# Kernel tuning notes

Measured on AMD Instinct MI355X. Metric: run time of the kernel, lower is better.

The kernel has to match this reference:

```python
import jax, jax.numpy as jnp
import numpy as np

D_MODEL = 1024
N_HEADS = 16
D_K = D_MODEL // N_HEADS
NEG = -1e9


def setup_inputs() -> dict:
    key = jax.random.key(0)
    ks = jax.random.split(key, 10)
    B, S = 4, 2048
    x = jax.random.normal(ks[0], (B, S, D_MODEL), dtype=jnp.float32)
    mask = jax.random.randint(ks[1], (B, S, S), 0, 2).astype(jnp.bool_)
    sc = 1.0 / np.sqrt(D_MODEL)
    Wq = jax.random.normal(ks[2], (D_MODEL, D_MODEL), dtype=jnp.float32) * sc
    bq = jnp.zeros((D_MODEL,), dtype=jnp.float32)
    Wk = jax.random.normal(ks[3], (D_MODEL, D_MODEL), dtype=jnp.float32) * sc
    bk = jnp.zeros((D_MODEL,), dtype=jnp.float32)
    Wv = jax.random.normal(ks[4], (D_MODEL, D_MODEL), dtype=jnp.float32) * sc
    bv = jnp.zeros((D_MODEL,), dtype=jnp.float32)
    Wo = jax.random.normal(ks[5], (D_MODEL, D_MODEL), dtype=jnp.float32) * sc
    bo = jnp.zeros((D_MODEL,), dtype=jnp.float32)
    return {"x": x, "mask": mask, "Wq": Wq, "bq": bq, "Wk": Wk, "bk": bk,
            "Wv": Wv, "bv": bv, "Wo": Wo, "bo": bo}


def _split_heads(t, B, S):
    # [B,S,d_model] -> [B,H,S,d_k]
    return t.reshape(B, S, N_HEADS, D_K).transpose(0, 2, 1, 3)


def reference(x, mask, Wq, bq, Wk, bk, Wv, bv, Wo, bo):
    B, S, _ = x.shape
    Q = _split_heads(x @ Wq + bq, B, S)
    K = _split_heads(x @ Wk + bk, B, S)
    V = _split_heads(x @ Wv + bv, B, S)
    scale = jnp.sqrt(jnp.float32(D_K))
    scores = jnp.einsum('bhqd,bhkd->bhqk', Q, K) / scale
    scores = jnp.where(mask[:, None, :, :], jnp.float32(NEG), scores)
    attn = jax.nn.softmax(scores, axis=-1)
    ctx = jnp.einsum('bhqk,bhkd->bhqd', attn, V)
    ctx = ctx.transpose(0, 2, 1, 3).reshape(B, S, D_MODEL)
    return ctx @ Wo + bo
```

## Files before the change

kernel.cpp:

```cpp
#include <hip/hip_runtime.h>

#define D_MODEL 1024
#define N_HEADS 16
#define D_K     64
#define BATCH   4
#define SEQ     2048
#define MROWS   (BATCH * SEQ)

typedef __bf16 bf16x8 __attribute__((ext_vector_type(8)));
typedef float  f32x4  __attribute__((ext_vector_type(4)));
typedef unsigned short ushort8 __attribute__((ext_vector_type(8)));
typedef unsigned short ushort4v __attribute__((ext_vector_type(4)));

__device__ inline unsigned short f2bf(float f) {
    union { float f; unsigned int u; } v; v.f = f;
    unsigned int u = v.u;
    unsigned int r = (u + 0x7fffu + ((u >> 16) & 1u)) >> 16;
    return (unsigned short)r;
}

__device__ inline void load_lds16(const void* g, void* l) {
    __builtin_amdgcn_global_load_lds(
        (const __attribute__((address_space(1))) unsigned int*)g,
        (__attribute__((address_space(3))) unsigned int*)l, 16, 0, 0);
}

__global__ __launch_bounds__(256) void wprep(const float* __restrict__ Wq,
                                             const float* __restrict__ Wk,
                                             const float* __restrict__ Wv,
                                             const float* __restrict__ Wo,
                                             unsigned short* __restrict__ wt) {
    __shared__ __align__(16) unsigned short t[64][65];
    int w  = blockIdx.z;
    const float* W = (w == 0) ? Wq : (w == 1) ? Wk : (w == 2) ? Wv : Wo;
    int k0 = blockIdx.x * 64, n0 = blockIdx.y * 64;
    int tid = threadIdx.x;
    int nl = tid & 63, kq = tid >> 6;
#pragma unroll
    for (int i = 0; i < 16; i++) {
        int kl = kq * 16 + i;
        t[kl][nl] = f2bf(W[(size_t)(k0 + kl) * D_MODEL + n0 + nl]);
    }
    __syncthreads();
    unsigned short* out = wt + (size_t)w * D_MODEL * D_MODEL;
#pragma unroll
    for (int p = 0; p < 2; p++) {
        int nrow = p * 32 + (tid >> 3);
        int c8   = (tid & 7) * 8;
        ushort8 o;
#pragma unroll
        for (int j = 0; j < 8; j++) o[j] = t[c8 + j][nrow];
        *reinterpret_cast<ushort8*>(out + (size_t)(n0 + nrow) * D_MODEL + k0 + c8) = o;
    }
}

__global__ __launch_bounds__(256) void xprep(const float4* __restrict__ x,
                                             unsigned short* __restrict__ xb) {
    int i = blockIdx.x * 256 + threadIdx.x;
    float4 v = x[i];
    ushort4v o;
    o[0] = f2bf(v.x); o[1] = f2bf(v.y); o[2] = f2bf(v.z); o[3] = f2bf(v.w);
    *reinterpret_cast<ushort4v*>(xb + (size_t)i * 4) = o;
}

__global__ __launch_bounds__(256) void mprep(const int* __restrict__ mask,
                                             unsigned long long* __restrict__ mb) {
    int row = blockIdx.x;
    int tid = threadIdx.x;
    int wv  = tid >> 6;
#pragma unroll
    for (int w = 0; w < 8; w++) {
        int col = w * 256 + tid;
        int mval = mask[(size_t)row * SEQ + col];
        unsigned long long bits = __ballot(mval != 0);
        if ((tid & 63) == 0) mb[(size_t)row * 32 + w * 4 + wv] = bits;
    }
}

__global__ __launch_bounds__(256) void qkv_gemm(const unsigned short* __restrict__ xb,
                                                const unsigned short* __restrict__ wt,
                                                const float* __restrict__ bq,
                                                const float* __restrict__ bk,
                                                const float* __restrict__ bvv,
                                                unsigned short* __restrict__ qb,
                                                unsigned short* __restrict__ kb,
                                                unsigned short* __restrict__ vt) {
    __shared__ __align__(16) unsigned short lds_a[128 * 32];
    __shared__ __align__(16) unsigned short lds_b[128 * 32];
    int tid = threadIdx.x;
    int wave = tid >> 6, lane = tid & 63;
    int c = lane & 15, g = lane >> 4;
    int wave_m = (wave & 1) * 64, wave_n = (wave >> 1) * 64;
    int nblk = blockIdx.x * 128, mblk = blockIdx.y * 128;

    int oct0 = wave * 128 + lane, oct1 = oct0 + 64;
    int ra0 = oct0 >> 2, ga0 = ((oct0 & 3) ^ (ra0 & 3)) * 8;
    int ra1 = oct1 >> 2, ga1 = ((oct1 & 3) ^ (ra1 & 3)) * 8;
    const unsigned short* pa0 = xb + (size_t)(mblk + ra0) * D_MODEL + ga0;
    const unsigned short* pa1 = xb + (size_t)(mblk + ra1) * D_MODEL + ga1;
    const unsigned short* pb0 = wt + (size_t)(nblk + ra0) * D_MODEL + ga0;
    const unsigned short* pb1 = wt + (size_t)(nblk + ra1) * D_MODEL + ga1;
    unsigned short* la0 = lds_a + wave * 1024;
    unsigned short* la1 = la0 + 512;
    unsigned short* lb0 = lds_b + wave * 1024;
    unsigned short* lb1 = lb0 + 512;

    int aoff[4], boff[4];
#pragma unroll
    for (int mi = 0; mi < 4; mi++) {
        int row = wave_m + mi * 16 + c;
        aoff[mi] = (row * 4 + (g ^ (row & 3))) * 16;
    }
#pragma unroll
    for (int ni = 0; ni < 4; ni++) {
        int row = wave_n + ni * 16 + c;
        boff[ni] = (row * 4 + (g ^ (row & 3))) * 16;
    }

    f32x4 acc[4][4];
#pragma unroll
    for (int mi = 0; mi < 4; mi++)
#pragma unroll
        for (int ni = 0; ni < 4; ni++) acc[mi][ni] = f32x4{0.f, 0.f, 0.f, 0.f};

    for (int k0 = 0; k0 < D_MODEL; k0 += 32) {
        load_lds16(pa0 + k0, la0);
        load_lds16(pa1 + k0, la1);
        load_lds16(pb0 + k0, lb0);
        load_lds16(pb1 + k0, lb1);
        __syncthreads();
        bf16x8 af[4], bfr[4];
#pragma unroll
        for (int mi = 0; mi < 4; mi++)
            af[mi] = *reinterpret_cast<const bf16x8*>(reinterpret_cast<const char*>(lds_a) + aoff[mi]);
#pragma unroll
        for (int ni = 0; ni < 4; ni++)
            bfr[ni] = *reinterpret_cast<const bf16x8*>(reinterpret_cast<const char*>(lds_b) + boff[ni]);
#pragma unroll
        for (int mi = 0; mi < 4; mi++)
#pragma unroll
            for (int ni = 0; ni < 4; ni++)
                acc[mi][ni] = __builtin_amdgcn_mfma_f32_16x16x32_bf16(af[mi], bfr[ni], acc[mi][ni], 0, 0, 0);
        __syncthreads();
    }

    int nb = nblk + wave_n;
    int wsel = nb >> 10;
    int h = (nb >> 6) & 15;
    int dk0 = nb & 63;
    int mglob = mblk + wave_m;
    int b = mglob >> 11;
    int s0 = mglob & (SEQ - 1);
    size_t bh = (size_t)(b * N_HEADS + h);
    const float* bias = (wsel == 0) ? bq : (wsel == 1) ? bk : bvv;
    int nn = nb & (D_MODEL - 1);
    float bval[4];
#pragma unroll
    for (int ni = 0; ni < 4; ni++) bval[ni] = bias[nn + ni * 16 + c];

    if (wsel < 2) {
        unsigned short* outp = wsel ? kb : qb;
#pragma unroll
        for (int mi = 0; mi < 4; mi++)
#pragma unroll
            for (int ni = 0; ni < 4; ni++) {
                int dk = dk0 + ni * 16 + c;
#pragma unroll
                for (int r = 0; r < 4; r++) {
                    int s = s0 + mi * 16 + g * 4 + r;
                    outp[(bh * SEQ + s) * 64 + dk] = f2bf(acc[mi][ni][r] + bval[ni]);
                }
            }
    } else {
#pragma unroll
        for (int mi = 0; mi < 4; mi++)
#pragma unroll
            for (int ni = 0; ni < 4; ni++) {
                int dk = dk0 + ni * 16 + c;
                int s = s0 + mi * 16 + g * 4;
                ushort4v o;
#pragma unroll
                for (int r = 0; r < 4; r++) o[r] = f2bf(acc[mi][ni][r] + bval[ni]);
                *reinterpret_cast<ushort4v*>(vt + (bh * 64 + dk) * SEQ + s) = o;
            }
    }
}

__global__ __launch_bounds__(256) void attn(const unsigned short* __restrict__ qb,
                                            const unsigned short* __restrict__ kb,
                                            const unsigned short* __restrict__ vt,
                                            const unsigned long long* __restrict__ mb,
                                            unsigned short* __restrict__ ctx) {
    __shared__ __align__(16) unsigned short lds_k[64 * 64];
    __shared__ __align__(16) unsigned short lds_v[64 * 64];
    __shared__ __align__(16) unsigned short lp[4][16][72];
    int tid = threadIdx.x;
    int wave = tid >> 6, lane = tid & 63;
    int c = lane & 15, g = lane >> 4;
    int bh = blockIdx.x >> 5;
    int q0 = (blockIdx.x & 31) * 64 + wave * 16;
    int b = bh >> 4;
    const unsigned short* qbase = qb + (size_t)bh * SEQ * 64;
    const unsigned short* kbase = kb + (size_t)bh * SEQ * 64;
    const unsigned short* vbase = vt + (size_t)bh * 64 * SEQ;
    const unsigned long long* mrow = mb + ((size_t)b * SEQ + q0 + g * 4) * 32;

    bf16x8 qf[2];
    qf[0] = *reinterpret_cast<const bf16x8*>(qbase + (size_t)(q0 + c) * 64 + g * 8);
    qf[1] = *reinterpret_cast<const bf16x8*>(qbase + (size_t)(q0 + c) * 64 + 32 + g * 8);

    int j0 = wave * 128 + lane, j1 = j0 + 64;
    int sr0 = j0 >> 3, so0 = (j0 & 7) ^ (sr0 & 7);
    int sr1 = j1 >> 3, so1 = (j1 & 7) ^ (sr1 & 7);
    const unsigned short* ks0 = kbase + (size_t)sr0 * 64 + so0 * 8;
    const unsigned short* ks1 = kbase + (size_t)sr1 * 64 + so1 * 8;
    const unsigned short* vs0 = vbase + (size_t)sr0 * SEQ + so0 * 8;
    const unsigned short* vs1 = vbase + (size_t)sr1 * SEQ + so1 * 8;
    unsigned short* lk0 = lds_k + wave * 1024;
    unsigned short* lk1 = lk0 + 512;
    unsigned short* lv0 = lds_v + wave * 1024;
    unsigned short* lv1 = lv0 + 512;

    int koff[4][2], voff[4][2];
#pragma unroll
    for (int st = 0; st < 4; st++) {
        int row = st * 16 + c;
#pragma unroll
        for (int kk = 0; kk < 2; kk++)
            koff[st][kk] = (row * 8 + ((kk * 4 + g) ^ (row & 7))) * 16;
    }
#pragma unroll
    for (int t = 0; t < 4; t++) {
        int row = t * 16 + c;
#pragma unroll
        for (int kk = 0; kk < 2; kk++)
            voff[t][kk] = (row * 8 + ((kk * 4 + g) ^ (row & 7))) * 16;
    }

    float lsum[4] = {0.f, 0.f, 0.f, 0.f};
    f32x4 po[4];
#pragma unroll
    for (int t = 0; t < 4; t++) po[t] = f32x4{0.f, 0.f, 0.f, 0.f};

    for (int key0 = 0; key0 < SEQ; key0 += 64) {
        load_lds16(ks0 + (size_t)key0 * 64, lk0);
        load_lds16(ks1 + (size_t)key0 * 64, lk1);
        load_lds16(vs0 + key0, lv0);
        load_lds16(vs1 + key0, lv1);
        unsigned long long wm[4];
#pragma unroll
        for (int r = 0; r < 4; r++) wm[r] = mrow[r * 32 + (key0 >> 6)];
        __syncthreads();

        f32x4 s[4];
#pragma unroll
        for (int st = 0; st < 4; st++) {
            s[st] = f32x4{0.f, 0.f, 0.f, 0.f};
            s[st] = __builtin_amdgcn_mfma_f32_16x16x32_bf16(
                qf[0], *reinterpret_cast<const bf16x8*>(reinterpret_cast<const char*>(lds_k) + koff[st][0]), s[st], 0, 0, 0);
            s[st] = __builtin_amdgcn_mfma_f32_16x16x32_bf16(
                qf[1], *reinterpret_cast<const bf16x8*>(reinterpret_cast<const char*>(lds_k) + koff[st][1]), s[st], 0, 0, 0);
        }
#pragma unroll
        for (int r = 0; r < 4; r++) {
            unsigned int lo = (unsigned int)wm[r];
            unsigned int hi = (unsigned int)(wm[r] >> 32);
#pragma unroll
            for (int st = 0; st < 4; st++) {
                unsigned int w32 = (st < 2) ? lo : hi;
                unsigned int bit = (w32 >> ((st & 1) * 16 + c)) & 1u;
                float p = bit ? 0.f : __expf(s[st][r] * 0.125f);
                lsum[r] += p;
                lp[wave][g * 4 + r][st * 16 + c] = f2bf(p);
            }
        }
        bf16x8 pf0 = *reinterpret_cast<const bf16x8*>(&lp[wave][c][g * 8]);
        bf16x8 pf1 = *reinterpret_cast<const bf16x8*>(&lp[wave][c][32 + g * 8]);
#pragma unroll
        for (int t = 0; t < 4; t++) {
            po[t] = __builtin_amdgcn_mfma_f32_16x16x32_bf16(
                pf0, *reinterpret_cast<const bf16x8*>(reinterpret_cast<const char*>(lds_v) + voff[t][0]), po[t], 0, 0, 0);
            po[t] = __builtin_amdgcn_mfma_f32_16x16x32_bf16(
                pf1, *reinterpret_cast<const bf16x8*>(reinterpret_cast<const char*>(lds_v) + voff[t][1]), po[t], 0, 0, 0);
        }
        __syncthreads();
    }

    float inv[4];
#pragma unroll
    for (int r = 0; r < 4; r++) {
        float l = lsum[r];
        l += __shfl_xor(l, 1);
        l += __shfl_xor(l, 2);
        l += __shfl_xor(l, 4);
        l += __shfl_xor(l, 8);
        inv[r] = 1.f / l;
    }
    int h = bh & 15;
#pragma unroll
    for (int t = 0; t < 4; t++)
#pragma unroll
        for (int r = 0; r < 4; r++) {
            int row = g * 4 + r;
            ctx[((size_t)b * SEQ + q0 + row) * D_MODEL + h * 64 + t * 16 + c] = f2bf(po[t][r] * inv[r]);
        }
}

__global__ __launch_bounds__(256) void oproj(const unsigned short* __restrict__ ctx,
                                             const unsigned short* __restrict__ wt,
                                             const float* __restrict__ bo,
                                             float* __restrict__ out) {
    __shared__ __align__(16) unsigned short lds_a[128 * 32];
    __shared__ __align__(16) unsigned short lds_b[128 * 32];
    int tid = threadIdx.x;
    int wave = tid >> 6, lane = tid & 63;
    int c = lane & 15, g = lane >> 4;
    int wave_m = (wave & 1) * 64, wave_n = (wave >> 1) * 64;
    int nblk = blockIdx.x * 128, mblk = blockIdx.y * 128;
    const unsigned short* wo = wt + (size_t)3 * D_MODEL * D_MODEL;

    int oct0 = wave * 128 + lane, oct1 = oct0 + 64;
    int ra0 = oct0 >> 2, ga0 = ((oct0 & 3) ^ (ra0 & 3)) * 8;
    int ra1 = oct1 >> 2, ga1 = ((oct1 & 3) ^ (ra1 & 3)) * 8;
    const unsigned short* pa0 = ctx + (size_t)(mblk + ra0) * D_MODEL + ga0;
    const unsigned short* pa1 = ctx + (size_t)(mblk + ra1) * D_MODEL + ga1;
    const unsigned short* pb0 = wo + (size_t)(nblk + ra0) * D_MODEL + ga0;
    const unsigned short* pb1 = wo + (size_t)(nblk + ra1) * D_MODEL + ga1;
    unsigned short* la0 = lds_a + wave * 1024;
    unsigned short* la1 = la0 + 512;
    unsigned short* lb0 = lds_b + wave * 1024;
    unsigned short* lb1 = lb0 + 512;

    int aoff[4], boff[4];
#pragma unroll
    for (int mi = 0; mi < 4; mi++) {
        int row = wave_m + mi * 16 + c;
        aoff[mi] = (row * 4 + (g ^ (row & 3))) * 16;
    }
#pragma unroll
    for (int ni = 0; ni < 4; ni++) {
        int row = wave_n + ni * 16 + c;
        boff[ni] = (row * 4 + (g ^ (row & 3))) * 16;
    }

    f32x4 acc[4][4];
#pragma unroll
    for (int mi = 0; mi < 4; mi++)
#pragma unroll
        for (int ni = 0; ni < 4; ni++) acc[mi][ni] = f32x4{0.f, 0.f, 0.f, 0.f};

    for (int k0 = 0; k0 < D_MODEL; k0 += 32) {
        load_lds16(pa0 + k0, la0);
        load_lds16(pa1 + k0, la1);
        load_lds16(pb0 + k0, lb0);
        load_lds16(pb1 + k0, lb1);
        __syncthreads();
        bf16x8 af[4], bfr[4];
#pragma unroll
        for (int mi = 0; mi < 4; mi++)
            af[mi] = *reinterpret_cast<const bf16x8*>(reinterpret_cast<const char*>(lds_a) + aoff[mi]);
#pragma unroll
        for (int ni = 0; ni < 4; ni++)
            bfr[ni] = *reinterpret_cast<const bf16x8*>(reinterpret_cast<const char*>(lds_b) + boff[ni]);
#pragma unroll
        for (int mi = 0; mi < 4; mi++)
#pragma unroll
            for (int ni = 0; ni < 4; ni++)
                acc[mi][ni] = __builtin_amdgcn_mfma_f32_16x16x32_bf16(af[mi], bfr[ni], acc[mi][ni], 0, 0, 0);
        __syncthreads();
    }

    float bval[4];
#pragma unroll
    for (int ni = 0; ni < 4; ni++) bval[ni] = bo[nblk + wave_n + ni * 16 + c];
#pragma unroll
    for (int mi = 0; mi < 4; mi++)
#pragma unroll
        for (int ni = 0; ni < 4; ni++) {
            int n = nblk + wave_n + ni * 16 + c;
#pragma unroll
            for (int r = 0; r < 4; r++) {
                int m = mblk + wave_m + mi * 16 + g * 4 + r;
                out[(size_t)m * D_MODEL + n] = acc[mi][ni][r] + bval[ni];
            }
        }
}

extern "C" void kernel_launch(void* const* d_in, const int* in_sizes, int n_in,
                              void* d_out, int out_size, void* d_ws, size_t ws_size,
                              hipStream_t stream) {
    const float* x    = (const float*)d_in[0];
    const int*   mask = (const int*)d_in[1];
    const float* Wq = (const float*)d_in[2];
    const float* bq = (const float*)d_in[3];
    const float* Wk = (const float*)d_in[4];
    const float* bk = (const float*)d_in[5];
    const float* Wv = (const float*)d_in[6];
    const float* bv = (const float*)d_in[7];
    const float* Wo = (const float*)d_in[8];
    const float* bo = (const float*)d_in[9];
    float* out = (float*)d_out;

    char* ws = (char*)d_ws;
    const size_t MB = 1024 * 1024;
    unsigned short* wt  = (unsigned short*)(ws + 0 * MB);
    unsigned short* xb  = (unsigned short*)(ws + 8 * MB);
    unsigned short* qb  = (unsigned short*)(ws + 24 * MB);
    unsigned short* kb  = (unsigned short*)(ws + 40 * MB);
    unsigned short* vt  = (unsigned short*)(ws + 56 * MB);
    unsigned short* ctx = (unsigned short*)(ws + 72 * MB);
    unsigned long long* mb = (unsigned long long*)(ws + 88 * MB);

    wprep<<<dim3(16, 16, 4), 256, 0, stream>>>(Wq, Wk, Wv, Wo, wt);
    xprep<<<dim3(MROWS * D_MODEL / 4 / 256), 256, 0, stream>>>((const float4*)x, xb);
    mprep<<<dim3(MROWS), 256, 0, stream>>>(mask, mb);
    qkv_gemm<<<dim3(24, 64), 256, 0, stream>>>(xb, wt, bq, bk, bv, qb, kb, vt);
    attn<<<dim3(2048), 256, 0, stream>>>(qb, kb, vt, mb, ctx);
    oproj<<<dim3(8, 64), 256, 0, stream>>>(ctx, wt, bo, out);
}
```

Measured before the change: 408.8 us.

## Double-buffer K/V tiles in attention and compute transposed scores for cheaper masking

Double-buffers the K and V LDS tiles so the next key block's global-to-LDS loads are issued while the current block is computed, dropping one barrier per iteration. The QK^T MFMA operands are swapped so each lane holds a single query row, which lets one 64-bit mask word per lane be used and the mask applied with bitwise ops instead of branches. Probabilities are packed into bf16 by truncation (no rounding) and written as 8-byte stores, and the row-sum reduction is restructured. This uses twice the K/V LDS, which may lower occupancy, and slightly changes numerics through truncation.

After: 412.9 us. Within noise of the previous version (+1.0%).

```diff
diff --git a/kernel.cpp b/kernel.cpp
--- a/kernel.cpp
+++ b/kernel.cpp
@@ -191,8 +191,8 @@
                                             const unsigned short* __restrict__ vt,
                                             const unsigned long long* __restrict__ mb,
                                             unsigned short* __restrict__ ctx) {
-    __shared__ __align__(16) unsigned short lds_k[64 * 64];
-    __shared__ __align__(16) unsigned short lds_v[64 * 64];
+    __shared__ __align__(16) unsigned short lds_k[2][64 * 64];
+    __shared__ __align__(16) unsigned short lds_v[2][64 * 64];
     __shared__ __align__(16) unsigned short lp[4][16][72];
     int tid = threadIdx.x;
     int wave = tid >> 6, lane = tid & 63;
@@ -203,11 +203,10 @@
     const unsigned short* qbase = qb + (size_t)bh * SEQ * 64;
     const unsigned short* kbase = kb + (size_t)bh * SEQ * 64;
     const unsigned short* vbase = vt + (size_t)bh * 64 * SEQ;
-    const unsigned long long* mrow = mb + ((size_t)b * SEQ + q0 + g * 4) * 32;
-
-    bf16x8 qf[2];
-    qf[0] = *reinterpret_cast<const bf16x8*>(qbase + (size_t)(q0 + c) * 64 + g * 8);
-    qf[1] = *reinterpret_cast<const bf16x8*>(qbase + (size_t)(q0 + c) * 64 + 32 + g * 8);
+    const unsigned long long* mrowp = mb + ((size_t)b * SEQ + q0 + c) * 32;
+
+    bf16x8 qf0 = *reinterpret_cast<const bf16x8*>(qbase + (size_t)(q0 + c) * 64 + g * 8);
+    bf16x8 qf1 = *reinterpret_cast<const bf16x8*>(qbase + (size_t)(q0 + c) * 64 + 32 + g * 8);
 
     int j0 = wave * 128 + lane, j1 = j0 + 64;
     int sr0 = j0 >> 3, so0 = (j0 & 7) ^ (sr0 & 7);
@@ -216,10 +215,6 @@
     const unsigned short* ks1 = kbase + (size_t)sr1 * 64 + so1 * 8;
     const unsigned short* vs0 = vbase + (size_t)sr0 * SEQ + so0 * 8;
     const unsigned short* vs1 = vbase + (size_t)sr1 * SEQ + so1 * 8;
-    unsigned short* lk0 = lds_k + wave * 1024;
-    unsigned short* lk1 = lk0 + 512;
-    unsigned short* lv0 = lds_v + wave * 1024;
-    unsigned short* lv1 = lv0 + 512;
 
     int koff[4][2], voff[4][2];
 #pragma unroll
@@ -237,72 +232,89 @@
             voff[t][kk] = (row * 8 + ((kk * 4 + g) ^ (row & 7))) * 16;
     }
 
-    float lsum[4] = {0.f, 0.f, 0.f, 0.f};
+    load_lds16(ks0, &lds_k[0][wave * 1024]);
+    load_lds16(ks1, &lds_k[0][wave * 1024 + 512]);
+    load_lds16(vs0, &lds_v[0][wave * 1024]);
+    load_lds16(vs1, &lds_v[0][wave * 1024 + 512]);
+    unsigned long long wcur = mrowp[0];
+
+    float lsum = 0.f;
     f32x4 po[4];
 #pragma unroll
     for (int t = 0; t < 4; t++) po[t] = f32x4{0.f, 0.f, 0.f, 0.f};
 
-    for (int key0 = 0; key0 < SEQ; key0 += 64) {
-        load_lds16(ks0 + (size_t)key0 * 64, lk0);
-        load_lds16(ks1 + (size_t)key0 * 64, lk1);
-        load_lds16(vs0 + key0, lv0);
-        load_lds16(vs1 + key0, lv1);
-        unsigned long long wm[4];
-#pragma unroll
-        for (int r = 0; r < 4; r++) wm[r] = mrow[r * 32 + (key0 >> 6)];
+    for (int it = 0; it < SEQ / 64; it++) {
+        int cur = it & 1;
         __syncthreads();
+        if (it + 1 < SEQ / 64) {
+            int nxt = cur ^ 1;
+            int key0n = (it + 1) * 64;
+            load_lds16(ks0 + (size_t)key0n * 64, &lds_k[nxt][wave * 1024]);
+            load_lds16(ks1 + (size_t)key0n * 64, &lds_k[nxt][wave * 1024 + 512]);
+            load_lds16(vs0 + key0n, &lds_v[nxt][wave * 1024]);
+            load_lds16(vs1 + key0n, &lds_v[nxt][wave * 1024 + 512]);
+        }
+        unsigned long long wnx = (it + 1 < SEQ / 64) ? mrowp[it + 1] : 0ull;
+        const char* lk = reinterpret_cast<const char*>(&lds_k[cur][0]);
+        const char* lv = reinterpret_cast<const char*>(&lds_v[cur][0]);
 
         f32x4 s[4];
 #pragma unroll
         for (int st = 0; st < 4; st++) {
             s[st] = f32x4{0.f, 0.f, 0.f, 0.f};
             s[st] = __builtin_amdgcn_mfma_f32_16x16x32_bf16(
-                qf[0], *reinterpret_cast<const bf16x8*>(reinterpret_cast<const char*>(lds_k) + koff[st][0]), s[st], 0, 0, 0);
+                *reinterpret_cast<const bf16x8*>(lk + koff[st][0]), qf0, s[st], 0, 0, 0);
             s[st] = __builtin_amdgcn_mfma_f32_16x16x32_bf16(
-                qf[1], *reinterpret_cast<const bf16x8*>(reinterpret_cast<const char*>(lds_k) + koff[st][1]), s[st], 0, 0, 0);
-        }
-#pragma unroll
-        for (int r = 0; r < 4; r++) {
-            unsigned int lo = (unsigned int)wm[r];
-            unsigned int hi = (unsigned int)(wm[r] >> 32);
-#pragma unroll
-            for (int st = 0; st < 4; st++) {
-                unsigned int w32 = (st < 2) ? lo : hi;
-                unsigned int bit = (w32 >> ((st & 1) * 16 + c)) & 1u;
-                float p = bit ? 0.f : __expf(s[st][r] * 0.125f);
-                lsum[r] += p;
-                lp[wave][g * 4 + r][st * 16 + c] = f2bf(p);
+                *reinterpret_cast<const bf16x8*>(lk + koff[st][1]), qf1, s[st], 0, 0, 0);
+        }
+
+        unsigned int a0 = ~(unsigned int)wcur;
+        unsigned int a1 = ~(unsigned int)(wcur >> 32);
+        wcur = wnx;
+#pragma unroll
+        for (int st = 0; st < 4; st++) {
+            unsigned int aw = (st < 2) ? a0 : a1;
+            int base = 31 - ((st & 1) << 4) - g * 4;
+            unsigned int pt[4];
+#pragma unroll
+            for (int r = 0; r < 4; r++) {
+                unsigned int m2 = (unsigned int)((int)(aw << (base - r)) >> 31) & 0xFFFF0000u;
+                float p = __expf(s[st][r] * 0.125f);
+                unsigned int tt = __float_as_uint(p) & m2;
+                lsum += __uint_as_float(tt);
+                pt[r] = tt;
             }
-        }
+            uint2 u;
+            u.x = (pt[0] >> 16) | pt[1];
+            u.y = (pt[2] >> 16) | pt[3];
+            *reinterpret_cast<uint2*>(&lp[wave][c][st * 16 + g * 4]) = u;
+        }
+
         bf16x8 pf0 = *reinterpret_cast<const bf16x8*>(&lp[wave][c][g * 8]);
         bf16x8 pf1 = *reinterpret_cast<const bf16x8*>(&lp[wave][c][32 + g * 8]);
 #pragma unroll
         for (int t = 0; t < 4; t++) {
             po[t] = __builtin_amdgcn_mfma_f32_16x16x32_bf16(
-                pf0, *reinterpret_cast<const bf16x8*>(reinterpret_cast<const char*>(lds_v) + voff[t][0]), po[t], 0, 0, 0);
+                pf0, *reinterpret_cast<const bf16x8*>(lv + voff[t][0]), po[t], 0, 0, 0);
             po[t] = __builtin_amdgcn_mfma_f32_16x16x32_bf16(
-                pf1, *reinterpret_cast<const bf16x8*>(reinterpret_cast<const char*>(lds_v) + voff[t][1]), po[t], 0, 0, 0);
-        }
-        __syncthreads();
-    }
-
-    float inv[4];
-#pragma unroll
-    for (int r = 0; r < 4; r++) {
-        float l = lsum[r];
-        l += __shfl_xor(l, 1);
-        l += __shfl_xor(l, 2);
-        l += __shfl_xor(l, 4);
-        l += __shfl_xor(l, 8);
-        inv[r] = 1.f / l;
-    }
+                pf1, *reinterpret_cast<const bf16x8*>(lv + voff[t][1]), po[t], 0, 0, 0);
+        }
+    }
+
+    lsum += __shfl_xor(lsum, 16);
+    lsum += __shfl_xor(lsum, 32);
+    float invr[4];
+#pragma unroll
+    for (int r = 0; r < 4; r++)
+        invr[r] = 1.f / __shfl(lsum, g * 4 + r);
+
     int h = bh & 15;
 #pragma unroll
     for (int t = 0; t < 4; t++)
 #pragma unroll
         for (int r = 0; r < 4; r++) {
             int row = g * 4 + r;
-            ctx[((size_t)b * SEQ + q0 + row) * D_MODEL + h * 64 + t * 16 + c] = f2bf(po[t][r] * inv[r]);
+            ctx[((size_t)b * SEQ + q0 + row) * D_MODEL + h * 64 + t * 16 + c] = f2bf(po[t][r] * invr[r]);
         }
 }
 
```
